# Kernel tuning notes

Hardware: AMD Instinct MI355X
Metric: run time of the kernel (lower is better)

## Reference

```python
import jax, jax.numpy as jnp
import numpy as np

N_IMG = 1024
N_VIEWS = 90


def _bilinear(img, yi, xi):
    """Bilinear sample img at float coords (yi=row, xi=col); 0 outside (skimage warp cval=0)."""
    n = img.shape[0]
    y0 = jnp.floor(yi)
    x0 = jnp.floor(xi)
    wy = yi - y0
    wx = xi - x0
    y0i = y0.astype(jnp.int32)
    x0i = x0.astype(jnp.int32)

    def get(yy, xx):
        valid = (yy >= 0) & (yy < n) & (xx >= 0) & (xx < n)
        v = img[jnp.clip(yy, 0, n - 1), jnp.clip(xx, 0, n - 1)]
        return jnp.where(valid, v, jnp.zeros((), img.dtype))

    v00 = get(y0i, x0i)
    v01 = get(y0i, x0i + 1)
    v10 = get(y0i + 1, x0i)
    v11 = get(y0i + 1, x0i + 1)
    return (v00 * (1 - wy) * (1 - wx) + v01 * (1 - wy) * wx
            + v10 * wy * (1 - wx) + v11 * wy * wx)


def radon_jax(image, theta_deg):
    """skimage.transform.radon(image, theta, circle=True) equivalent.
    Rotate image by each angle (bilinear, about center = N//2, inverse map as in
    skimage warp) and sum over rows. Returns sinogram [N, n_angles]."""
    n = image.shape[0]
    center = n // 2
    ang = jnp.deg2rad(theta_deg.astype(image.dtype))
    cos_a = jnp.cos(ang)  # [A]
    sin_a = jnp.sin(ang)
    coords = jnp.arange(n, dtype=image.dtype)
    X, Y = jnp.meshgrid(coords, coords)  # X = col (x), Y = row (y), [N, N]

    def rotate_and_sum(ca, sa):
        # inverse map: src = R @ dst (homogeneous, (x, y) order) as in skimage radon
        x_in = ca * X + sa * Y - center * (ca + sa - 1)
        y_in = -sa * X + ca * Y - center * (ca - sa - 1)
        rotated = _bilinear(image, y_in, x_in)  # [N, N]
        return rotated.sum(axis=0)  # sum over rows -> projection [N]

    sino = jax.vmap(rotate_and_sum)(cos_a, sin_a)  # [A, N]
    return sino.T  # [N, A] to match skimage radon layout


def setup_inputs() -> dict:
    key = jax.random.key(0)
    k1, _ = jax.random.split(key)
    x = jax.random.normal(k1, (N_IMG, N_IMG), dtype=jnp.float32)
    theta = jnp.arange(N_VIEWS, dtype=jnp.float32) * 2.0  # 0..178 deg, 2-deg spacing
    return {"x": x, "theta": theta}


def reference(x, theta):
    return radon_jax(x, theta)
```

## Files before the change

kernel.cpp:

```cpp
#include <hip/hip_runtime.h>

#define N_IMG   1024
#define N_VIEWS 90
#define CENTER  512
#define TILE    64
#define NYB     (N_IMG / TILE)
#define NTHREADS 512
#define NWAVES   8
#define YPT      (TILE / NWAVES)
#define TILE_WORDS 9216

typedef float v2f __attribute__((ext_vector_type(2)));

__device__ __forceinline__ void map_coords(float ca, float sa, float cx, float cy,
                                           float Xf, float Yf,
                                           float& x_in, float& y_in) {
    const float fx0 = fmaf(ca, Xf, cx);
    const float fy0 = fmaf(-sa, Xf, cy);
    x_in = fmaf(sa, Yf, fx0);
    y_in = fmaf(ca, Yf, fy0);
}

__device__ __forceinline__ void gload_lds4(const float* g, float* l) {
    __builtin_amdgcn_global_load_lds((const __attribute__((address_space(1))) void*)g,
                                     (__attribute__((address_space(3))) void*)l, 4, 0, 0);
}
__device__ __forceinline__ void gload_lds16(const float* g, float* l) {
    __builtin_amdgcn_global_load_lds((const __attribute__((address_space(1))) void*)g,
                                     (__attribute__((address_space(3))) void*)l, 16, 0, 0);
}

template<int STRIDE>
__device__ __forceinline__ float sample_tile(const float* __restrict__ tile,
                                             float sa, float ca,
                                             float x_in, float y_in, float basef) {
    const float Sf = (float)STRIDE;
    v2f x2 = {x_in, x_in + sa};
    v2f y2 = {y_in, y_in + ca};
    const v2f dx2 = {2.0f * sa, 2.0f * sa};
    const v2f dy2 = {2.0f * ca, 2.0f * ca};
    const v2f S2  = {Sf, Sf};
    const v2f b2  = {basef, basef};
    v2f acc2 = {0.0f, 0.0f};
    #pragma unroll
    for (int p = 0; p < YPT / 2; ++p) {
        v2f x0f = {floorf(x2.x), floorf(x2.y)};
        v2f y0f = {floorf(y2.x), floorf(y2.y)};
        const v2f wx = x2 - x0f;
        const v2f wy = y2 - y0f;
        const v2f lif = y0f * S2 + x0f + b2;
        const int li0 = (int)lif.x;
        const int li1 = (int)lif.y;
        const v2f t00 = {tile[li0],              tile[li1]};
        const v2f t01 = {tile[li0 + 1],          tile[li1 + 1]};
        const v2f t10 = {tile[li0 + STRIDE],     tile[li1 + STRIDE]};
        const v2f t11 = {tile[li0 + STRIDE + 1], tile[li1 + STRIDE + 1]};
        const v2f top = (t01 - t00) * wx + t00;
        const v2f bot = (t11 - t10) * wx + t10;
        acc2 += (bot - top) * wy + top;
        x2 += dx2; y2 += dy2;
    }
    return acc2.x + acc2.y;
}

__global__ __launch_bounds__(NTHREADS) void radon_tile(const float* __restrict__ img,
                                                       const float* __restrict__ theta,
                                                       float* __restrict__ partial,
                                                       float* __restrict__ out,
                                                       int mode) {
    __shared__ float tile[TILE_WORDS];
    __shared__ float fpar[4];
    __shared__ int   ipar[8];

    const int a  = blockIdx.z;
    const int X0 = blockIdx.x * TILE;
    const int Y0 = blockIdx.y * TILE;
    const int tid  = threadIdx.x;
    const int lane = tid & 63;
    const int wv   = tid >> 6;

    if (wv == 0) {
        const float ang = theta[a] * 0.017453292519943295f;
        float sa, ca;
        __sincosf(ang, &sa, &ca);
        const float cx = (float)CENTER * (1.0f - ca - sa);
        const float cy = (float)CENTER * (1.0f - ca + sa);

        float x00, y00, x01, y01, x10, y10, x11, y11;
        map_coords(ca, sa, cx, cy, (float)X0,        (float)Y0,        x00, y00);
        map_coords(ca, sa, cx, cy, (float)(X0 + 63), (float)Y0,        x01, y01);
        map_coords(ca, sa, cx, cy, (float)X0,        (float)(Y0 + 63), x10, y10);
        map_coords(ca, sa, cx, cy, (float)(X0 + 63), (float)(Y0 + 63), x11, y11);
        const float xmin = fminf(fminf(x00, x01), fminf(x10, x11));
        const float xmax = fmaxf(fmaxf(x00, x01), fmaxf(x10, x11));
        const float ymin = fminf(fminf(y00, y01), fminf(y10, y11));
        const float ymax = fmaxf(fmaxf(y00, y01), fmaxf(y10, y11));

        const int ix0_raw = (int)floorf(xmin);
        const int ix1_raw = (int)floorf(xmax) + 1;
        const int iy0_raw = (int)floorf(ymin);
        const int iy1_raw = (int)floorf(ymax) + 1;

        const bool empty = (ix1_raw < 0) || (ix0_raw > N_IMG - 1) ||
                           (iy1_raw < 0) || (iy0_raw > N_IMG - 1);
        const bool interior = (ix0_raw >= 0) && (ix1_raw <= N_IMG - 1) &&
                              (iy0_raw >= 0) && (iy1_raw <= N_IMG - 1);

        int path = (fabsf(ca) > 0.7072f) ? 0 : ((ca > 0.0f) ? 1 : 2);
        int iy0w, win, dB = 0, ry0 = 0, nrows = 0;
        if (interior) {
            iy0w = iy0_raw;
            if (path == 0) {
                win = min(ix0_raw & ~3, N_IMG - 96);
            } else {
                win = min(ix0_raw, N_IMG - 64);
                dB  = max(win, ix1_raw - 63) - win;
            }
            nrows = iy1_raw - iy0_raw + 1;
        } else {
            iy0w = iy0_raw;
            win  = ix0_raw & ~3;
            ry0  = max(0, iy0_raw);
            nrows = min(N_IMG - 1, iy1_raw) - ry0 + 1;
        }
        if (tid == 0) {
            fpar[0] = sa; fpar[1] = ca; fpar[2] = cx; fpar[3] = cy;
            ipar[0] = iy0w; ipar[1] = nrows; ipar[2] = win; ipar[3] = dB;
            ipar[4] = path;
            ipar[5] = empty ? 1 : (interior ? 2 : 0);
            ipar[6] = ry0;
        }
    }
    __syncthreads();

    float* __restrict__ pslot = partial + ((size_t)(a * NYB + blockIdx.y) << 10) + X0;
    const int flags = ipar[5];

    if (flags & 1) {
        if (mode == 0 && tid < 64) pslot[tid] = 0.0f;
        return;
    }

    const float sa = fpar[0], ca = fpar[1], cx = fpar[2], cy = fpar[3];
    const int iy0 = ipar[0], nrows = ipar[1], win = ipar[2], dB = ipar[3];
    const int path = ipar[4];
    const int S = (path == 0) ? 96 : ((path == 1) ? 95 : 97);

    if (flags & 2) {
        if (path == 0) {
            const int D = nrows * 96;
            for (int o = wv * 256; o < D; o += NWAVES * 256) {
                const int d = o + 4 * lane;
                const int r = (unsigned)d / 96u;
                const int c = d - r * 96;
                const int gr = min(iy0 + r, N_IMG - 1);
                gload_lds16(img + (size_t)gr * N_IMG + win + c, tile + o);
            }
        } else {
            const float* g = img + (size_t)(iy0 + wv) * N_IMG + win + lane;
            float* l = tile + wv * S;
            for (int r = wv; r < nrows; r += NWAVES) {
                gload_lds4(g, l);
                if (dB > 0) gload_lds4(g + dB, l + dB);
                g += NWAVES * N_IMG;
                l += NWAVES * S;
            }
        }
    } else {
        for (int o4 = tid; o4 < TILE_WORDS / 4; o4 += NTHREADS)
            *(float4*)(tile + 4 * o4) = make_float4(0.f, 0.f, 0.f, 0.f);
        __syncthreads();
        const int ry0 = ipar[6];
        const int cx0 = max(0, win);
        const int cxe = min(N_IMG - 1, win + 94);
        const int wIn = cxe - cx0 + 1;
        const int n4  = wIn >> 2;
        const int items = nrows * 24;
        for (int idx = tid; idx < items; idx += NTHREADS) {
            const int r  = (unsigned)idx / 24u;
            const int c4 = idx - r * 24;
            const int gy = ry0 + r;
            float* dst = tile + (gy - iy0) * S + (cx0 - win) + 4 * c4;
            const float* src = img + (size_t)gy * N_IMG + cx0 + 4 * c4;
            if (c4 < n4) {
                *(float4*)dst = *(const float4*)src;
            } else if (c4 == n4) {
                for (int j = 0; j < (wIn & 3); ++j) dst[j] = src[j];
            }
        }
    }
    __syncthreads();

    const float Xf  = (float)(X0 + lane);
    const float fx0 = fmaf(ca, Xf, cx);
    const float fy0 = fmaf(-sa, Xf, cy);
    const float Ybf = (float)(Y0 + wv * YPT);
    const float x_in = fmaf(sa, Ybf, fx0);
    const float y_in = fmaf(ca, Ybf, fy0);
    const float basef = -(float)(iy0 * S + win);

    float acc;
    if (path == 0)      acc = sample_tile<96>(tile, sa, ca, x_in, y_in, basef);
    else if (path == 1) acc = sample_tile<95>(tile, sa, ca, x_in, y_in, basef);
    else                acc = sample_tile<97>(tile, sa, ca, x_in, y_in, basef);

    __syncthreads();
    tile[wv * 64 + lane] = acc;
    __syncthreads();
    if (wv == 0) {
        float s = 0.0f;
        #pragma unroll
        for (int w = 0; w < NWAVES; ++w) s += tile[w * 64 + lane];
        if (mode == 0) pslot[lane] = s;
        else           atomicAdd(&out[(X0 + lane) * N_VIEWS + a], s);
    }
}

__global__ __launch_bounds__(256) void reduce_partials(const float* __restrict__ partial,
                                                       float* __restrict__ out) {
    const int g = blockIdx.x * 256 + threadIdx.x;
    const int a = g >> 10;
    const int X = g & 1023;
    float s = 0.0f;
    #pragma unroll
    for (int yb = 0; yb < NYB; ++yb)
        s += partial[((size_t)(a * NYB + yb) << 10) + X];
    out[X * N_VIEWS + a] = s;
}

extern "C" void kernel_launch(void* const* d_in, const int* in_sizes, int n_in,
                              void* d_out, int out_size, void* d_ws, size_t ws_size,
                              hipStream_t stream) {
    const float* img   = (const float*)d_in[0];
    const float* theta = (const float*)d_in[1];
    float* out     = (float*)d_out;
    float* partial = (float*)d_ws;

    const size_t needed = (size_t)N_VIEWS * NYB * N_IMG * sizeof(float);
    const int mode = (ws_size >= needed) ? 0 : 1;
    if (mode == 1)
        hipMemsetAsync(d_out, 0, (size_t)out_size * sizeof(float), stream);

    dim3 grid(N_IMG / TILE, N_IMG / TILE, N_VIEWS);
    radon_tile<<<grid, NTHREADS, 0, stream>>>(img, theta, partial, out, mode);

    if (mode == 0)
        reduce_partials<<<(N_VIEWS * N_IMG) / 256, 256, 0, stream>>>(partial, out);
}
```

Baseline: 140.5 us.

## Loop each block over eight Y tiles and accumulate via atomics, dropping partials pass

Each block now walks 8 consecutive 64-row tiles in a column strip, accumulating projections in registers. Parameters for the next tile are computed while the current tile loads, using a double-buffered parameter array. The partial-sum workspace and separate reduce kernel are replaced by a memset and 2 atomic adds per output element. This removes a kernel launch and the partial traffic, at the cost of 8x fewer blocks, serialized per-tile load/sample phases with extra barriers, and float atomics that make the summation order nondeterministic.

```diff
diff --git a/kernel.cpp b/kernel.cpp
--- a/kernel.cpp
+++ b/kernel.cpp
@@ -4,13 +4,11 @@
 #define N_VIEWS 90
 #define CENTER  512
 #define TILE    64
-#define NYB     (N_IMG / TILE)
+#define NTPB    8
 #define NTHREADS 512
 #define NWAVES   8
 #define YPT      (TILE / NWAVES)
 #define TILE_WORDS 9216
-
-typedef float v2f __attribute__((ext_vector_type(2)));
 
 __device__ __forceinline__ void map_coords(float ca, float sa, float cx, float cy,
                                            float Xf, float Yf,
@@ -29,6 +27,8 @@
     __builtin_amdgcn_global_load_lds((const __attribute__((address_space(1))) void*)g,
                                      (__attribute__((address_space(3))) void*)l, 16, 0, 0);
 }
+
+typedef float v2f __attribute__((ext_vector_type(2)));
 
 template<int STRIDE>
 __device__ __forceinline__ float sample_tile(const float* __restrict__ tile,
@@ -63,18 +63,60 @@
     return acc2.x + acc2.y;
 }
 
+__device__ __forceinline__ void compute_params(int* dst, int X0, int Y0,
+                                               float sa, float ca, float cx, float cy,
+                                               bool store) {
+    float x00, y00, x01, y01, x10, y10, x11, y11;
+    map_coords(ca, sa, cx, cy, (float)X0,        (float)Y0,        x00, y00);
+    map_coords(ca, sa, cx, cy, (float)(X0 + 63), (float)Y0,        x01, y01);
+    map_coords(ca, sa, cx, cy, (float)X0,        (float)(Y0 + 63), x10, y10);
+    map_coords(ca, sa, cx, cy, (float)(X0 + 63), (float)(Y0 + 63), x11, y11);
+    const float xmin = fminf(fminf(x00, x01), fminf(x10, x11));
+    const float xmax = fmaxf(fmaxf(x00, x01), fmaxf(x10, x11));
+    const float ymin = fminf(fminf(y00, y01), fminf(y10, y11));
+    const float ymax = fmaxf(fmaxf(y00, y01), fmaxf(y10, y11));
+
+    const int ix0_raw = (int)floorf(xmin);
+    const int ix1_raw = (int)floorf(xmax) + 1;
+    const int iy0_raw = (int)floorf(ymin);
+    const int iy1_raw = (int)floorf(ymax) + 1;
+
+    const bool empty = (ix1_raw < 0) || (ix0_raw > N_IMG - 1) ||
+                       (iy1_raw < 0) || (iy0_raw > N_IMG - 1);
+    const bool interior = (ix0_raw >= 0) && (ix1_raw <= N_IMG - 1) &&
+                          (iy0_raw >= 0) && (iy1_raw <= N_IMG - 1);
+
+    int path = (fabsf(ca) > 0.7072f) ? 0 : ((ca > 0.0f) ? 1 : 2);
+    int iy0w = iy0_raw, win = 0, dB = 0, ry0 = 0, nrows = 0;
+    if (interior) {
+        if (path == 0) {
+            win = min(ix0_raw & ~3, N_IMG - 96);
+        } else {
+            win = min(ix0_raw, N_IMG - 64);
+            dB  = max(win, ix1_raw - 63) - win;
+        }
+        nrows = iy1_raw - iy0_raw + 1;
+    } else {
+        win  = ix0_raw & ~3;
+        ry0  = max(0, iy0_raw);
+        nrows = min(N_IMG - 1, iy1_raw) - ry0 + 1;
+    }
+    if (store) {
+        dst[0] = iy0w; dst[1] = nrows; dst[2] = win; dst[3] = dB;
+        dst[4] = path; dst[5] = empty ? 1 : (interior ? 2 : 0); dst[6] = ry0;
+    }
+}
+
 __global__ __launch_bounds__(NTHREADS) void radon_tile(const float* __restrict__ img,
                                                        const float* __restrict__ theta,
-                                                       float* __restrict__ partial,
-                                                       float* __restrict__ out,
-                                                       int mode) {
+                                                       float* __restrict__ out) {
     __shared__ float tile[TILE_WORDS];
     __shared__ float fpar[4];
-    __shared__ int   ipar[8];
+    __shared__ int   ipar[2][8];
 
     const int a  = blockIdx.z;
     const int X0 = blockIdx.x * TILE;
-    const int Y0 = blockIdx.y * TILE;
+    const int tb = blockIdx.y * NTPB;
     const int tid  = threadIdx.x;
     const int lane = tid & 63;
     const int wv   = tid >> 6;
@@ -85,147 +127,97 @@
         __sincosf(ang, &sa, &ca);
         const float cx = (float)CENTER * (1.0f - ca - sa);
         const float cy = (float)CENTER * (1.0f - ca + sa);
-
-        float x00, y00, x01, y01, x10, y10, x11, y11;
-        map_coords(ca, sa, cx, cy, (float)X0,        (float)Y0,        x00, y00);
-        map_coords(ca, sa, cx, cy, (float)(X0 + 63), (float)Y0,        x01, y01);
-        map_coords(ca, sa, cx, cy, (float)X0,        (float)(Y0 + 63), x10, y10);
-        map_coords(ca, sa, cx, cy, (float)(X0 + 63), (float)(Y0 + 63), x11, y11);
-        const float xmin = fminf(fminf(x00, x01), fminf(x10, x11));
-        const float xmax = fmaxf(fmaxf(x00, x01), fmaxf(x10, x11));
-        const float ymin = fminf(fminf(y00, y01), fminf(y10, y11));
-        const float ymax = fmaxf(fmaxf(y00, y01), fmaxf(y10, y11));
-
-        const int ix0_raw = (int)floorf(xmin);
-        const int ix1_raw = (int)floorf(xmax) + 1;
-        const int iy0_raw = (int)floorf(ymin);
-        const int iy1_raw = (int)floorf(ymax) + 1;
-
-        const bool empty = (ix1_raw < 0) || (ix0_raw > N_IMG - 1) ||
-                           (iy1_raw < 0) || (iy0_raw > N_IMG - 1);
-        const bool interior = (ix0_raw >= 0) && (ix1_raw <= N_IMG - 1) &&
-                              (iy0_raw >= 0) && (iy1_raw <= N_IMG - 1);
-
-        int path = (fabsf(ca) > 0.7072f) ? 0 : ((ca > 0.0f) ? 1 : 2);
-        int iy0w, win, dB = 0, ry0 = 0, nrows = 0;
-        if (interior) {
-            iy0w = iy0_raw;
-            if (path == 0) {
-                win = min(ix0_raw & ~3, N_IMG - 96);
-            } else {
-                win = min(ix0_raw, N_IMG - 64);
-                dB  = max(win, ix1_raw - 63) - win;
-            }
-            nrows = iy1_raw - iy0_raw + 1;
-        } else {
-            iy0w = iy0_raw;
-            win  = ix0_raw & ~3;
-            ry0  = max(0, iy0_raw);
-            nrows = min(N_IMG - 1, iy1_raw) - ry0 + 1;
-        }
-        if (tid == 0) {
-            fpar[0] = sa; fpar[1] = ca; fpar[2] = cx; fpar[3] = cy;
-            ipar[0] = iy0w; ipar[1] = nrows; ipar[2] = win; ipar[3] = dB;
-            ipar[4] = path;
-            ipar[5] = empty ? 1 : (interior ? 2 : 0);
-            ipar[6] = ry0;
-        }
+        if (tid == 0) { fpar[0] = sa; fpar[1] = ca; fpar[2] = cx; fpar[3] = cy; }
+        compute_params(ipar[0], X0, tb * TILE, sa, ca, cx, cy, tid == 0);
     }
     __syncthreads();
 
-    float* __restrict__ pslot = partial + ((size_t)(a * NYB + blockIdx.y) << 10) + X0;
-    const int flags = ipar[5];
-
-    if (flags & 1) {
-        if (mode == 0 && tid < 64) pslot[tid] = 0.0f;
-        return;
-    }
-
     const float sa = fpar[0], ca = fpar[1], cx = fpar[2], cy = fpar[3];
-    const int iy0 = ipar[0], nrows = ipar[1], win = ipar[2], dB = ipar[3];
-    const int path = ipar[4];
-    const int S = (path == 0) ? 96 : ((path == 1) ? 95 : 97);
-
-    if (flags & 2) {
-        if (path == 0) {
-            const int D = nrows * 96;
-            for (int o = wv * 256; o < D; o += NWAVES * 256) {
-                const int d = o + 4 * lane;
-                const int r = (unsigned)d / 96u;
-                const int c = d - r * 96;
-                const int gr = min(iy0 + r, N_IMG - 1);
-                gload_lds16(img + (size_t)gr * N_IMG + win + c, tile + o);
-            }
-        } else {
-            const float* g = img + (size_t)(iy0 + wv) * N_IMG + win + lane;
-            float* l = tile + wv * S;
-            for (int r = wv; r < nrows; r += NWAVES) {
-                gload_lds4(g, l);
-                if (dB > 0) gload_lds4(g + dB, l + dB);
-                g += NWAVES * N_IMG;
-                l += NWAVES * S;
-            }
-        }
-    } else {
-        for (int o4 = tid; o4 < TILE_WORDS / 4; o4 += NTHREADS)
-            *(float4*)(tile + 4 * o4) = make_float4(0.f, 0.f, 0.f, 0.f);
-        __syncthreads();
-        const int ry0 = ipar[6];
-        const int cx0 = max(0, win);
-        const int cxe = min(N_IMG - 1, win + 94);
-        const int wIn = cxe - cx0 + 1;
-        const int n4  = wIn >> 2;
-        const int items = nrows * 24;
-        for (int idx = tid; idx < items; idx += NTHREADS) {
-            const int r  = (unsigned)idx / 24u;
-            const int c4 = idx - r * 24;
-            const int gy = ry0 + r;
-            float* dst = tile + (gy - iy0) * S + (cx0 - win) + 4 * c4;
-            const float* src = img + (size_t)gy * N_IMG + cx0 + 4 * c4;
-            if (c4 < n4) {
-                *(float4*)dst = *(const float4*)src;
-            } else if (c4 == n4) {
-                for (int j = 0; j < (wIn & 3); ++j) dst[j] = src[j];
-            }
-        }
-    }
-    __syncthreads();
-
     const float Xf  = (float)(X0 + lane);
     const float fx0 = fmaf(ca, Xf, cx);
     const float fy0 = fmaf(-sa, Xf, cy);
-    const float Ybf = (float)(Y0 + wv * YPT);
-    const float x_in = fmaf(sa, Ybf, fx0);
-    const float y_in = fmaf(ca, Ybf, fy0);
-    const float basef = -(float)(iy0 * S + win);
-
-    float acc;
-    if (path == 0)      acc = sample_tile<96>(tile, sa, ca, x_in, y_in, basef);
-    else if (path == 1) acc = sample_tile<95>(tile, sa, ca, x_in, y_in, basef);
-    else                acc = sample_tile<97>(tile, sa, ca, x_in, y_in, basef);
-
-    __syncthreads();
+
+    float acc = 0.0f;
+
+    #pragma unroll 1
+    for (int t = 0; t < NTPB; ++t) {
+        const int* P = ipar[t & 1];
+        const int iy0 = P[0], nrows = P[1], win = P[2], dB = P[3];
+        const int path = P[4], flags = P[5], ry0 = P[6];
+        const int S = (path == 0) ? 96 : ((path == 1) ? 95 : 97);
+
+        if (!(flags & 1)) {
+            if (flags & 2) {
+                if (path == 0) {
+                    const int D = nrows * 96;
+                    for (int o = wv * 256; o < D; o += NWAVES * 256) {
+                        const int d = o + 4 * lane;
+                        const int r = (unsigned)d / 96u;
+                        const int c = d - r * 96;
+                        const int gr = min(iy0 + r, N_IMG - 1);
+                        gload_lds16(img + (size_t)gr * N_IMG + win + c, tile + o);
+                    }
+                } else {
+                    const float* g = img + (size_t)(iy0 + wv) * N_IMG + win + lane;
+                    float* l = tile + wv * S;
+                    for (int r = wv; r < nrows; r += NWAVES) {
+                        gload_lds4(g, l);
+                        if (dB > 0) gload_lds4(g + dB, l + dB);
+                        g += NWAVES * N_IMG;
+                        l += NWAVES * S;
+                    }
+                }
+            } else {
+                for (int o4 = tid; o4 < TILE_WORDS / 4; o4 += NTHREADS)
+                    *(float4*)(tile + 4 * o4) = make_float4(0.f, 0.f, 0.f, 0.f);
+                __syncthreads();
+                const int cx0 = max(0, win);
+                const int cxe = min(N_IMG - 1, win + 94);
+                const int wIn = cxe - cx0 + 1;
+                const int n4  = wIn >> 2;
+                const int items = nrows * 24;
+                for (int idx = tid; idx < items; idx += NTHREADS) {
+                    const int r  = (unsigned)idx / 24u;
+                    const int c4 = idx - r * 24;
+                    const int gy = ry0 + r;
+                    float* dst = tile + (gy - iy0) * S + (cx0 - win) + 4 * c4;
+                    const float* src = img + (size_t)gy * N_IMG + cx0 + 4 * c4;
+                    if (c4 < n4) {
+                        *(float4*)dst = *(const float4*)src;
+                    } else if (c4 == n4) {
+                        for (int j = 0; j < (wIn & 3); ++j) dst[j] = src[j];
+                    }
+                }
+            }
+        }
+
+        if (wv == 0 && t + 1 < NTPB)
+            compute_params(ipar[(t + 1) & 1], X0, (tb + t + 1) * TILE,
+                           sa, ca, cx, cy, tid == 0);
+
+        __syncthreads();
+
+        if (!(flags & 1)) {
+            const float Ybf = (float)((tb + t) * TILE + wv * YPT);
+            const float x_in = fmaf(sa, Ybf, fx0);
+            const float y_in = fmaf(ca, Ybf, fy0);
+            const float basef = -(float)(iy0 * S + win);
+            if (path == 0)      acc += sample_tile<96>(tile, sa, ca, x_in, y_in, basef);
+            else if (path == 1) acc += sample_tile<95>(tile, sa, ca, x_in, y_in, basef);
+            else                acc += sample_tile<97>(tile, sa, ca, x_in, y_in, basef);
+        }
+
+        __syncthreads();
+    }
+
     tile[wv * 64 + lane] = acc;
     __syncthreads();
     if (wv == 0) {
         float s = 0.0f;
         #pragma unroll
         for (int w = 0; w < NWAVES; ++w) s += tile[w * 64 + lane];
-        if (mode == 0) pslot[lane] = s;
-        else           atomicAdd(&out[(X0 + lane) * N_VIEWS + a], s);
-    }
-}
-
-__global__ __launch_bounds__(256) void reduce_partials(const float* __restrict__ partial,
-                                                       float* __restrict__ out) {
-    const int g = blockIdx.x * 256 + threadIdx.x;
-    const int a = g >> 10;
-    const int X = g & 1023;
-    float s = 0.0f;
-    #pragma unroll
-    for (int yb = 0; yb < NYB; ++yb)
-        s += partial[((size_t)(a * NYB + yb) << 10) + X];
-    out[X * N_VIEWS + a] = s;
+        atomicAdd(&out[(size_t)(X0 + lane) * N_VIEWS + a], s);
+    }
 }
 
 extern "C" void kernel_launch(void* const* d_in, const int* in_sizes, int n_in,
@@ -233,17 +225,10 @@
                               hipStream_t stream) {
     const float* img   = (const float*)d_in[0];
     const float* theta = (const float*)d_in[1];
-    float* out     = (float*)d_out;
-    float* partial = (float*)d_ws;
-
-    const size_t needed = (size_t)N_VIEWS * NYB * N_IMG * sizeof(float);
-    const int mode = (ws_size >= needed) ? 0 : 1;
-    if (mode == 1)
-        hipMemsetAsync(d_out, 0, (size_t)out_size * sizeof(float), stream);
-
-    dim3 grid(N_IMG / TILE, N_IMG / TILE, N_VIEWS);
-    radon_tile<<<grid, NTHREADS, 0, stream>>>(img, theta, partial, out, mode);
-
-    if (mode == 0)
-        reduce_partials<<<(N_VIEWS * N_IMG) / 256, 256, 0, stream>>>(partial, out);
-}
+    float* out = (float*)d_out;
+
+    (void)hipMemsetAsync(d_out, 0, (size_t)out_size * sizeof(float), stream);
+
+    dim3 grid(N_IMG / TILE, (N_IMG / TILE) / NTPB, N_VIEWS);
+    radon_tile<<<grid, NTHREADS, 0, stream>>>(img, theta, out);
+}
```

After: 145.4 us. +3.5%, slower.
